# Kernel optimization log

Hardware: AMD Instinct MI355X
Metric: run time of the kernel (lower is better)

## Reference

```python
import jax, jax.numpy as jnp
import numpy as np

B, L, H, W, C = 8, 512, 768, 12, 25
S = L * W          # span_idx count, reshaped to [B, L, W, H]
Hh = H // 2        # per-direction LSTM hidden (bidirectional)


def setup_inputs() -> dict:
    key = jax.random.key(0)
    ks = jax.random.split(key, 24)
    p = lambda k, shape: jax.random.normal(k, shape, jnp.float32) * 0.02
    z = lambda n: jnp.zeros((n,), jnp.float32)
    return {
        "we": jax.random.normal(ks[0], (B, L, H), jnp.float32),
        "mask": jnp.ones((B, L), jnp.int32),
        "span_idx": jax.random.randint(ks[1], (B, S, 2), 0, L, jnp.int32),
        "pe": jax.random.normal(ks[2], (B, C, H), jnp.float32),
        # BiLSTM params (PyTorch gate order i,f,g,o)
        "w_ih_f": p(ks[3], (4 * Hh, H)), "w_hh_f": p(ks[4], (4 * Hh, Hh)),
        "b_ih_f": z(4 * Hh), "b_hh_f": z(4 * Hh),
        "w_ih_b": p(ks[5], (4 * Hh, H)), "w_hh_b": p(ks[6], (4 * Hh, Hh)),
        "b_ih_b": z(4 * Hh), "b_hh_b": z(4 * Hh),
        # project_start MLP: H -> 4H -> H
        "start_w1": p(ks[7], (4 * H, H)), "start_b1": z(4 * H),
        "start_w2": p(ks[8], (H, 4 * H)), "start_b2": z(H),
        # project_end MLP
        "end_w1": p(ks[9], (4 * H, H)), "end_b1": z(4 * H),
        "end_w2": p(ks[10], (H, 4 * H)), "end_b2": z(H),
        # out_project MLP: 2H -> 4H -> H
        "out_w1": p(ks[11], (4 * H, 2 * H)), "out_b1": z(4 * H),
        "out_w2": p(ks[12], (H, 4 * H)), "out_b2": z(H),
        # prompt_proj MLP: H -> 4H -> H
        "pr_w1": p(ks[13], (4 * H, H)), "pr_b1": z(4 * H),
        "pr_w2": p(ks[14], (H, 4 * H)), "pr_b2": z(H),
    }


def lstm_dir(x, w_ih, w_hh, b_ih, b_hh, reverse):
    # x: [B,L,D] -> per-direction hidden sequence [B,L,Hh]
    xg = jnp.einsum('bld,gd->blg', x, w_ih) + b_ih  # precomputed input gates
    n = w_hh.shape[1]

    def step(carry, xg_t):
        h, c = carry
        g = xg_t + h @ w_hh.T + b_hh
        i, f, gg, o = jnp.split(g, 4, axis=-1)
        c = jax.nn.sigmoid(f) * c + jax.nn.sigmoid(i) * jnp.tanh(gg)
        h = jax.nn.sigmoid(o) * jnp.tanh(c)
        return (h, c), h

    init = (jnp.zeros((x.shape[0], n), x.dtype), jnp.zeros((x.shape[0], n), x.dtype))
    _, hs = jax.lax.scan(step, init, jnp.swapaxes(xg, 0, 1), reverse=reverse)
    return jnp.swapaxes(hs, 0, 1)


def mlp(x, w1, b1, w2, b2):
    # Linear -> ReLU -> (Dropout: identity in eval) -> Linear
    return jax.nn.relu(x @ w1.T + b1) @ w2.T + b2


def extract_elements(t, idx):
    # t: [B,L,D], idx: [B,S] -> [B,S,D]; indices clamped like torch
    idx = jnp.clip(idx, 0, t.shape[1] - 1)
    return jnp.take_along_axis(t, idx[..., None], axis=1)


def reference(we, mask, span_idx, pe,
              w_ih_f, w_hh_f, b_ih_f, b_hh_f,
              w_ih_b, w_hh_b, b_ih_b, b_hh_b,
              start_w1, start_b1, start_w2, start_b2,
              end_w1, end_b1, end_w2, end_b2,
              out_w1, out_b1, out_w2, out_b2,
              pr_w1, pr_b1, pr_w2, pr_b2):
    # 1) Bidirectional LSTM encoder (pad_packed zeros masked positions)
    hf = lstm_dir(we, w_ih_f, w_hh_f, b_ih_f, b_hh_f, reverse=False)
    hb = lstm_dir(we, w_ih_b, w_hh_b, b_ih_b, b_hh_b, reverse=True)
    h = jnp.concatenate([hf, hb], axis=-1) * mask[..., None].astype(we.dtype)
    # 2) SpanMarkerV0: dual MLP -> gather -> concat+relu -> out MLP
    start_rep = mlp(h, start_w1, start_b1, start_w2, start_b2)
    end_rep = mlp(h, end_w1, end_b1, end_w2, end_b2)
    ss = extract_elements(start_rep, span_idx[:, :, 0])
    es = extract_elements(end_rep, span_idx[:, :, 1])
    cat = jax.nn.relu(jnp.concatenate([ss, es], axis=-1))
    span = mlp(cat, out_w1, out_b1, out_w2, out_b2).reshape(B, L, W, H)
    # 3) Prompt projection
    prompt = mlp(pe, pr_w1, pr_b1, pr_w2, pr_b2)
    return (span, prompt)
```

## Files before the change

### kernel.cpp

```cpp
#include <hip/hip_runtime.h>
#include <hip/hip_bf16.h>
#include <stdint.h>

#define B_ 8
#define L_ 512
#define H_ 768
#define WW_ 12
#define C_ 25
#define S_ (L_*WW_)
#define HH 384
#define G4 1536

using bf16x8 = __attribute__((ext_vector_type(8))) short;
using f32x4  = __attribute__((ext_vector_type(4))) float;

static __device__ __forceinline__ unsigned short f2bf(float x){
  unsigned u = __float_as_uint(x);
  unsigned r = (u + 0x7FFFu + ((u >> 16) & 1u)) >> 16;
  return (unsigned short)r;
}
static __device__ __forceinline__ float bflo(unsigned u){ return __uint_as_float(u << 16); }
static __device__ __forceinline__ float bfhi(unsigned u){ return __uint_as_float(u & 0xFFFF0000u); }

static __device__ __forceinline__ float sigmoid_f(float x){
  x = fminf(15.f, fmaxf(-15.f, x));
  return 1.f / (1.f + __expf(-x));
}
static __device__ __forceinline__ float tanh_f(float x){
  x = fminf(15.f, fmaxf(-15.f, x));
  float e = __expf(-2.f * x);
  return (1.f - e) / (1.f + e);
}

static __device__ __forceinline__ void gl_lds16(const unsigned short* g, unsigned short* l){
  __builtin_amdgcn_global_load_lds(
      (const __attribute__((address_space(1))) unsigned int*)g,
      (__attribute__((address_space(3))) unsigned int*)l,
      16, 0, 0);
}

struct CastArgs {
  const float* s[14];
  unsigned short* d[14];
  long cum[15];
};

__global__ __launch_bounds__(256) void k_cast_multi(CastArgs a, long total){
  long i = (long)blockIdx.x * blockDim.x + threadIdx.x;
  if (i >= total) return;
  int seg = 0;
  while (i >= a.cum[seg + 1]) seg++;
  long j = i - a.cum[seg];
  float4 v = reinterpret_cast<const float4*>(a.s[seg])[j];
  ushort4 o;
  o.x = f2bf(v.x); o.y = f2bf(v.y); o.z = f2bf(v.z); o.w = f2bf(v.w);
  reinterpret_cast<ushort4*>(a.d[seg])[j] = o;
}

__global__ void k_biascomb(const float* __restrict__ a, const float* __restrict__ b,
                           float* __restrict__ o, int n){
  int i = blockIdx.x * blockDim.x + threadIdx.x;
  if (i < n) o[i] = a[i] + b[i];
}

template<int ACT, int OUTBF, int GX = 0>
__global__ __launch_bounds__(256) void k_gemm2(
    const unsigned short* __restrict__ A, const unsigned short* __restrict__ Bm,
    const float* __restrict__ bias, void* __restrict__ Cout,
    int M, int N, int K, int lda, int ldb)
{
  __shared__ unsigned short Al[128 * 64];
  __shared__ unsigned short Bl[128 * 64];

  const int tid  = threadIdx.x;
  const int lane = tid & 63;
  const int wave = tid >> 6;
  const int wr = wave >> 1, wc = wave & 1;
  const int l16 = lane & 15, lq = lane >> 4;
  const int m0 = (GX == 0 ? blockIdx.y : blockIdx.x) * 128;
  const int n0 = (GX == 0 ? blockIdx.x : blockIdx.y) * 128;

  const int r_ = tid >> 3;
  const int p_ = tid & 7;
  const int cS = ((p_ ^ (r_ & 7)) * 8);
  const unsigned short* Asrc[4];
  const unsigned short* Bsrc[4];
  #pragma unroll
  for (int i = 0; i < 4; i++){
    int ra = m0 + i * 32 + r_; ra = ra < M ? ra : (M - 1);
    Asrc[i] = A + (size_t)ra * lda + cS;
    int rb = n0 + i * 32 + r_; rb = rb < N ? rb : (N - 1);
    Bsrc[i] = Bm + (size_t)rb * ldb + cS;
  }

  f32x4 acc[4][4];
  #pragma unroll
  for (int a = 0; a < 4; a++)
    #pragma unroll
    for (int b = 0; b < 4; b++)
      acc[a][b] = (f32x4)0.f;

  const int sw0 = ((0 * 4 + lq) ^ (l16 & 7)) * 16;
  const int sw1 = ((1 * 4 + lq) ^ (l16 & 7)) * 16;
  const int aBase = (wr * 64 + l16) * 128;
  const int bBase = (wc * 64 + l16) * 128;

  for (int k0 = 0; k0 < K; k0 += 64){
    #pragma unroll
    for (int i = 0; i < 4; i++)
      gl_lds16(Asrc[i] + k0, Al + i * 2048 + tid * 8);
    #pragma unroll
    for (int i = 0; i < 4; i++)
      gl_lds16(Bsrc[i] + k0, Bl + i * 2048 + tid * 8);
    __syncthreads();

    #pragma unroll
    for (int kk = 0; kk < 2; kk++){
      const int sw = kk ? sw1 : sw0;
      bf16x8 av[4], bv[4];
      #pragma unroll
      for (int mi = 0; mi < 4; mi++)
        av[mi] = *reinterpret_cast<const bf16x8*>((const char*)Al + aBase + mi * 2048 + sw);
      #pragma unroll
      for (int ni = 0; ni < 4; ni++)
        bv[ni] = *reinterpret_cast<const bf16x8*>((const char*)Bl + bBase + ni * 2048 + sw);
      #pragma unroll
      for (int mi = 0; mi < 4; mi++)
        #pragma unroll
        for (int ni = 0; ni < 4; ni++)
          acc[mi][ni] = __builtin_amdgcn_mfma_f32_16x16x32_bf16(av[mi], bv[ni], acc[mi][ni], 0, 0, 0);
    }
    __syncthreads();
  }

  #pragma unroll
  for (int mi = 0; mi < 4; mi++){
    #pragma unroll
    for (int r = 0; r < 4; r++){
      int row = m0 + wr * 64 + mi * 16 + lq * 4 + r;
      if (row >= M) continue;
      #pragma unroll
      for (int ni = 0; ni < 4; ni++){
        int col = n0 + wc * 64 + ni * 16 + l16;
        float v = acc[mi][ni][r] + bias[col];
        if (ACT) v = v > 0.f ? v : 0.f;
        if (OUTBF) ((unsigned short*)Cout)[(size_t)row * N + col] = f2bf(v);
        else       ((float*)Cout)[(size_t)row * N + col] = v;
      }
    }
  }
}

__global__ __launch_bounds__(256) void k_gout(
    const unsigned short* __restrict__ Ps, const unsigned short* __restrict__ Pe,
    const int* __restrict__ sidx, const float* __restrict__ b1,
    const unsigned short* __restrict__ Bw, const float* __restrict__ b2,
    float* __restrict__ out)
{
  __shared__ unsigned short Al[128 * 64];
  __shared__ unsigned short Bl[128 * 64];
  __shared__ int idx2[128][2];

  const int tid  = threadIdx.x;
  const int lane = tid & 63;
  const int wave = tid >> 6;
  const int wr = wave >> 1, wc = wave & 1;
  const int l16 = lane & 15, lq = lane >> 4;

  const int wg   = blockIdx.x;
  const int xcd  = wg & 7;
  const int slot = wg >> 3;
  const int nblk = slot % 6;
  const int tm   = xcd + 8 * (slot / 6);
  const int b  = tm / 48;
  const int s0 = (tm % 48) * 128;
  const int n0 = nblk * 128;

  if (tid < 128){
    int s = s0 + tid;
    int i0 = sidx[((size_t)b * S_ + s) * 2 + 0];
    int i1 = sidx[((size_t)b * S_ + s) * 2 + 1];
    idx2[tid][0] = min(max(i0, 0), L_ - 1);
    idx2[tid][1] = min(max(i1, 0), L_ - 1);
  }
  __syncthreads();

  const int r_ = tid >> 3;
  const int p_ = tid & 7;
  const int cS = ((p_ ^ (r_ & 7)) * 8);
  const unsigned short* Bsrc[4];
  const unsigned short* As0[4];
  const unsigned short* As1[4];
  #pragma unroll
  for (int i = 0; i < 4; i++){
    Bsrc[i] = Bw + (size_t)(n0 + i * 32 + r_) * 3072 + cS;
    int rr = i * 32 + r_;
    As0[i] = Ps + (size_t)(b * L_ + idx2[rr][0]) * 3072 + cS;
    As1[i] = Pe + (size_t)(b * L_ + idx2[rr][1]) * 3072 + cS;
  }

  f32x4 acc[4][4];
  #pragma unroll
  for (int a = 0; a < 4; a++)
    #pragma unroll
    for (int c = 0; c < 4; c++)
      acc[a][c] = (f32x4)0.f;

  const int sw0 = ((0 * 4 + lq) ^ (l16 & 7)) * 16;
  const int sw1 = ((1 * 4 + lq) ^ (l16 & 7)) * 16;
  const int aBase = (wr * 64 + l16) * 128;
  const int bBase = (wc * 64 + l16) * 128;

  uint4 vaR[4], veR[4];
  float4 bbR0, bbR1;
  #pragma unroll
  for (int i = 0; i < 4; i++){
    vaR[i] = *reinterpret_cast<const uint4*>(As0[i]);
    veR[i] = *reinterpret_cast<const uint4*>(As1[i]);
  }
  bbR0 = *reinterpret_cast<const float4*>(b1 + cS);
  bbR1 = *reinterpret_cast<const float4*>(b1 + cS + 4);

  for (int k0 = 0; k0 < 3072; k0 += 64){
    #pragma unroll
    for (int i = 0; i < 4; i++)
      gl_lds16(Bsrc[i] + k0, Bl + i * 2048 + tid * 8);

    #pragma unroll
    for (int i = 0; i < 4; i++){
      uint4 va = vaR[i];
      uint4 ve = veR[i];
      float f[8];
      f[0] = bflo(va.x) + bflo(ve.x) + bbR0.x; f[1] = bfhi(va.x) + bfhi(ve.x) + bbR0.y;
      f[2] = bflo(va.y) + bflo(ve.y) + bbR0.z; f[3] = bfhi(va.y) + bfhi(ve.y) + bbR0.w;
      f[4] = bflo(va.z) + bflo(ve.z) + bbR1.x; f[5] = bfhi(va.z) + bfhi(ve.z) + bbR1.y;
      f[6] = bflo(va.w) + bflo(ve.w) + bbR1.z; f[7] = bfhi(va.w) + bfhi(ve.w) + bbR1.w;
      unsigned short e[8];
      #pragma unroll
      for (int j = 0; j < 8; j++){ float v = f[j] > 0.f ? f[j] : 0.f; e[j] = f2bf(v); }
      uint4 rr;
      rr.x = (unsigned)e[0] | ((unsigned)e[1] << 16);
      rr.y = (unsigned)e[2] | ((unsigned)e[3] << 16);
      rr.z = (unsigned)e[4] | ((unsigned)e[5] << 16);
      rr.w = (unsigned)e[6] | ((unsigned)e[7] << 16);
      *reinterpret_cast<uint4*>(Al + i * 2048 + tid * 8) = rr;
    }

    if (k0 + 64 < 3072){
      #pragma unroll
      for (int i = 0; i < 4; i++){
        vaR[i] = *reinterpret_cast<const uint4*>(As0[i] + k0 + 64);
        veR[i] = *reinterpret_cast<const uint4*>(As1[i] + k0 + 64);
      }
      bbR0 = *reinterpret_cast<const float4*>(b1 + k0 + 64 + cS);
      bbR1 = *reinterpret_cast<const float4*>(b1 + k0 + 64 + cS + 4);
    }
    __syncthreads();

    #pragma unroll
    for (int kk = 0; kk < 2; kk++){
      const int sw = kk ? sw1 : sw0;
      bf16x8 av[4], bv[4];
      #pragma unroll
      for (int mi = 0; mi < 4; mi++)
        av[mi] = *reinterpret_cast<const bf16x8*>((const char*)Al + aBase + mi * 2048 + sw);
      #pragma unroll
      for (int ni = 0; ni < 4; ni++)
        bv[ni] = *reinterpret_cast<const bf16x8*>((const char*)Bl + bBase + ni * 2048 + sw);
      #pragma unroll
      for (int mi = 0; mi < 4; mi++)
        #pragma unroll
        for (int ni = 0; ni < 4; ni++)
          acc[mi][ni] = __builtin_amdgcn_mfma_f32_16x16x32_bf16(av[mi], bv[ni], acc[mi][ni], 0, 0, 0);
    }
    __syncthreads();
  }

  #pragma unroll
  for (int mi = 0; mi < 4; mi++){
    #pragma unroll
    for (int r = 0; r < 4; r++){
      size_t row = (size_t)tm * 128 + wr * 64 + mi * 16 + lq * 4 + r;
      #pragma unroll
      for (int ni = 0; ni < 4; ni++){
        int col = n0 + wc * 64 + ni * 16 + l16;
        out[row * 768 + col] = acc[mi][ni][r] + b2[col];
      }
    }
  }
}

static __device__ __forceinline__ unsigned long long ald8(const unsigned long long* p){
  return __hip_atomic_load(p, __ATOMIC_RELAXED, __HIP_MEMORY_SCOPE_AGENT);
}

__global__ __launch_bounds__(512, 2) void k_lstm7(
    const float* __restrict__ xgc,
    const unsigned short* __restrict__ Wbf,
    const int* __restrict__ mask,
    unsigned short* __restrict__ hbf,
    unsigned int* __restrict__ hg)
{
  const int dir  = blockIdx.x / 6;
  const int part = blockIdx.x % 6;
  const int tid  = threadIdx.x;
  const int lane = tid & 63;
  const int w    = tid >> 6;
  const int l16  = lane & 15, lq = lane >> 4;

  __shared__ alignas(16) unsigned short hls[8 * HH];
  __shared__ float gsl[256 * 9];

  const float* xg = xgc + dir * 1536;
  const unsigned short* Wg = Wbf + (size_t)dir * G4 * HH;
  unsigned int* hgd = hg + dir * 2 * (8 * HH);

  bf16x8 bfr0[12], bfr1[12];
  {
    int r0 = w * 32 + l16;
    int r1 = w * 32 + 16 + l16;
    int g0 = r0 >> 6, j0u = r0 & 63;
    int g1 = r1 >> 6, j1u = r1 & 63;
    const unsigned short* p0 = Wg + ((size_t)g0 * HH + part * 64 + j0u) * HH + lq * 8;
    const unsigned short* p1 = Wg + ((size_t)g1 * HH + part * 64 + j1u) * HH + lq * 8;
    #pragma unroll
    for (int kf = 0; kf < 12; kf++){
      bfr0[kf] = *reinterpret_cast<const bf16x8*>(p0 + kf * 32);
      bfr1[kf] = *reinterpret_cast<const bf16x8*>(p1 + kf * 32);
    }
  }

  if (tid < 384) reinterpret_cast<uint4*>(hls)[tid] = uint4{0,0,0,0};

  const int cb = tid >> 6;
  const int cj = tid & 63;
  const int cu = part * 64 + cj;
  float c_state = 0.f;

  const int w0  = tid * 6;
  const int rb  = w0 / HH;
  const int ru  = w0 % HH;

  float xi, xf, xgg, xo, mvf;
  {
    const int t0 = dir ? (L_ - 1) : 0;
    const float* xr = xgc + dir * 1536 + ((size_t)cb * L_ + t0) * 3072;
    xi = xr[cu]; xf = xr[HH + cu]; xgg = xr[2 * HH + cu]; xo = xr[3 * HH + cu];
    mvf = (float)mask[cb * L_ + t0];
  }

  __syncthreads();

  for (int s = 0; s < L_; s++){
    const int t = dir ? (L_ - 1 - s) : s;

    float nxi = 0.f, nxf = 0.f, nxg = 0.f, nxo = 0.f, nmv = 0.f;
    if (s + 1 < L_){
      const int tn = dir ? (L_ - 2 - s) : (s + 1);
      const float* xr = xg + ((size_t)cb * L_ + tn) * 3072;
      nxi = xr[cu]; nxf = xr[HH + cu]; nxg = xr[2 * HH + cu]; nxo = xr[3 * HH + cu];
      nmv = (float)mask[cb * L_ + tn];
    }

    if (s > 0){
      const unsigned long long tg = (unsigned long long)s;
      const unsigned long long* P =
        reinterpret_cast<const unsigned long long*>(hgd + ((s - 1) & 1) * (8 * HH) + w0);
      unsigned long long v0 = ald8(P), v1 = ald8(P + 1), v2 = ald8(P + 2);
      for (;;){
        bool ok0 = (((v0 >> 16) & 0xFFFFull) == tg) & ((v0 >> 48) == tg);
        bool ok1 = (((v1 >> 16) & 0xFFFFull) == tg) & ((v1 >> 48) == tg);
        bool ok2 = (((v2 >> 16) & 0xFFFFull) == tg) & ((v2 >> 48) == tg);
        if (ok0 & ok1 & ok2) break;
        v0 = ald8(P); v1 = ald8(P + 1); v2 = ald8(P + 2);
      }
      unsigned p01 = (unsigned)(v0 & 0xFFFFu) | ((unsigned)((v0 >> 32) & 0xFFFFu) << 16);
      unsigned p23 = (unsigned)(v1 & 0xFFFFu) | ((unsigned)((v1 >> 32) & 0xFFFFu) << 16);
      unsigned p45 = (unsigned)(v2 & 0xFFFFu) | ((unsigned)((v2 >> 32) & 0xFFFFu) << 16);
      *reinterpret_cast<unsigned*>((char*)hls + ((rb * 768 + (ru    ) * 2) ^ (rb << 4))) = p01;
      *reinterpret_cast<unsigned*>((char*)hls + ((rb * 768 + (ru + 2) * 2) ^ (rb << 4))) = p23;
      *reinterpret_cast<unsigned*>((char*)hls + ((rb * 768 + (ru + 4) * 2) ^ (rb << 4))) = p45;
    }
    __syncthreads();

    f32x4 acc0 = (f32x4)0.f, acc1 = (f32x4)0.f;
    const int arow = l16 & 7;
    #pragma unroll
    for (int kf = 0; kf < 12; kf++){
      int by = (arow * 768 + kf * 64 + lq * 16) ^ (arow << 4);
      bf16x8 a = *reinterpret_cast<const bf16x8*>((const char*)hls + by);
      acc0 = __builtin_amdgcn_mfma_f32_16x16x32_bf16(a, bfr0[kf], acc0, 0, 0, 0);
      acc1 = __builtin_amdgcn_mfma_f32_16x16x32_bf16(a, bfr1[kf], acc1, 0, 0, 0);
    }
    if (lq < 2){
      int n0r = w * 32 + l16;
      int n1r = w * 32 + 16 + l16;
      #pragma unroll
      for (int r = 0; r < 4; r++){
        gsl[n0r * 9 + lq * 4 + r] = acc0[r];
        gsl[n1r * 9 + lq * 4 + r] = acc1[r];
      }
    }
    __syncthreads();

    {
      float gi = gsl[(0 * 64 + cj) * 9 + cb] + xi;
      float gf = gsl[(1 * 64 + cj) * 9 + cb] + xf;
      float gg = gsl[(2 * 64 + cj) * 9 + cb] + xgg;
      float go = gsl[(3 * 64 + cj) * 9 + cb] + xo;
      c_state = sigmoid_f(gf) * c_state + sigmoid_f(gi) * tanh_f(gg);
      float h = sigmoid_f(go) * tanh_f(c_state);
      unsigned short hb = f2bf(h);
      *reinterpret_cast<unsigned short*>((char*)hls + ((cb * 768 + cu * 2) ^ (cb << 4))) = hb;
      unsigned word = ((unsigned)(s + 1) << 16) | (unsigned)hb;
      __hip_atomic_store(&hgd[(s & 1) * (8 * HH) + cb * HH + cu], word,
                         __ATOMIC_RELAXED, __HIP_MEMORY_SCOPE_AGENT);
      hbf[((size_t)cb * L_ + t) * H_ + dir * HH + cu] = f2bf(h * mvf);
    }

    xi = nxi; xf = nxf; xgg = nxg; xo = nxo; mvf = nmv;
  }
}

extern "C" void kernel_launch(void* const* d_in, const int* in_sizes, int n_in,
                              void* d_out, int out_size, void* d_ws, size_t ws_size,
                              hipStream_t stream)
{
  (void)in_sizes; (void)n_in; (void)out_size; (void)ws_size;
  const float* we     = (const float*)d_in[0];
  const int*   mask   = (const int*)  d_in[1];
  const int*   sidx   = (const int*)  d_in[2];
  const float* pe     = (const float*)d_in[3];
  const float* w_ih_f = (const float*)d_in[4];
  const float* w_hh_f = (const float*)d_in[5];
  const float* b_ih_f = (const float*)d_in[6];
  const float* b_hh_f = (const float*)d_in[7];
  const float* w_ih_b = (const float*)d_in[8];
  const float* w_hh_b = (const float*)d_in[9];
  const float* b_ih_b = (const float*)d_in[10];
  const float* b_hh_b = (const float*)d_in[11];
  const float* sw1 = (const float*)d_in[12]; const float* sb1 = (const float*)d_in[13];
  const float* sw2 = (const float*)d_in[14]; const float* sb2 = (const float*)d_in[15];
  const float* ew1 = (const float*)d_in[16]; const float* eb1 = (const float*)d_in[17];
  const float* ew2 = (const float*)d_in[18]; const float* eb2 = (const float*)d_in[19];
  const float* ow1 = (const float*)d_in[20]; const float* ob1 = (const float*)d_in[21];
  const float* ow2 = (const float*)d_in[22]; const float* ob2 = (const float*)d_in[23];
  const float* pw1 = (const float*)d_in[24]; const float* pb1 = (const float*)d_in[25];
  const float* pw2 = (const float*)d_in[26]; const float* pb2 = (const float*)d_in[27];

  char* wsp = (char*)d_ws; size_t off = 0;
  auto alloc = [&](size_t bytes) -> void* {
    void* p = wsp + off;
    off += (bytes + 255) & ~(size_t)255;
    return p;
  };

  unsigned short* we_bf  = (unsigned short*)alloc((size_t)4096*768*2);
  unsigned short* wihc_bf= (unsigned short*)alloc((size_t)3072*768*2);
  float* bcc   = (float*)alloc((size_t)3072*4);
  float* zerob = (float*)alloc((size_t)3072*4);
  float* sbe1  = (float*)alloc((size_t)6144*4);
  float* xgc   = (float*)alloc((size_t)4096*3072*4);
  unsigned short* whh_bf = (unsigned short*)alloc((size_t)2*1536*384*2);
  unsigned int* hg = (unsigned int*)alloc((size_t)2*2*8*384*4);
  unsigned short* h_bf  = (unsigned short*)alloc((size_t)4096*768*2);
  unsigned short* swe1b = (unsigned short*)alloc((size_t)6144*768*2);
  unsigned short* sw2b  = (unsigned short*)alloc((size_t)768*3072*2);
  unsigned short* ew2b  = (unsigned short*)alloc((size_t)768*3072*2);
  unsigned short* ow1b  = (unsigned short*)alloc((size_t)3072*1536*2);
  unsigned short* ow2b  = (unsigned short*)alloc((size_t)768*3072*2);
  unsigned short* pw1b  = (unsigned short*)alloc((size_t)3072*768*2);
  unsigned short* pw2b  = (unsigned short*)alloc((size_t)768*3072*2);
  unsigned short* srep  = (unsigned short*)alloc((size_t)4096*768*2);
  unsigned short* erep  = (unsigned short*)alloc((size_t)4096*768*2);
  unsigned short* midc  = (unsigned short*)alloc((size_t)4096*6144*2);
  unsigned short* pe_bf = (unsigned short*)alloc((size_t)200*768*2);
  unsigned short* pmid  = (unsigned short*)alloc((size_t)200*3072*2);

  unsigned short* Ps = (unsigned short*)xgc;
  unsigned short* Pe = (unsigned short*)xgc + (size_t)4096*3072;

  hipMemsetAsync(hg, 0, (size_t)2*2*8*384*4, stream);
  hipMemsetAsync(zerob, 0, (size_t)3072*4, stream);
  hipMemcpyAsync(sbe1,        sb1, (size_t)3072*4, hipMemcpyDeviceToDevice, stream);
  hipMemcpyAsync(sbe1 + 3072, eb1, (size_t)3072*4, hipMemcpyDeviceToDevice, stream);

  {
    CastArgs ca;
    const float* srcs[14] = { we, w_ih_f, w_ih_b, w_hh_f, w_hh_b, sw1, ew1,
                              sw2, ew2, ow1, ow2, pw1, pw2, pe };
    unsigned short* dsts[14] = { we_bf, wihc_bf, wihc_bf + 1536*768,
                                 whh_bf, whh_bf + 1536*384,
                                 swe1b, swe1b + 3072*768,
                                 sw2b, ew2b, ow1b, ow2b, pw1b, pw2b, pe_bf };
    long n4s[14] = { 4096L*768/4, 1536L*768/4, 1536L*768/4,
                     1536L*384/4, 1536L*384/4,
                     3072L*768/4, 3072L*768/4,
                     768L*3072/4, 768L*3072/4, 3072L*1536/4, 768L*3072/4,
                     3072L*768/4, 768L*3072/4, 200L*768/4 };
    long c = 0;
    for (int i = 0; i < 14; i++){ ca.s[i] = srcs[i]; ca.d[i] = dsts[i]; ca.cum[i] = c; c += n4s[i]; }
    ca.cum[14] = c;
    int grid = (int)((c + 255) / 256);
    k_cast_multi<<<grid, 256, 0, stream>>>(ca, c);
  }

  k_biascomb<<<6, 256, 0, stream>>>(b_ih_f, b_hh_f, bcc, 1536);
  k_biascomb<<<6, 256, 0, stream>>>(b_ih_b, b_hh_b, bcc + 1536, 1536);

  dim3 blk(256);
  k_gemm2<0,0><<<dim3(24, 32), blk, 0, stream>>>(we_bf, wihc_bf, bcc, xgc, 4096, 3072, 768, 768, 768);

  k_lstm7<<<12, 512, 0, stream>>>(xgc, whh_bf, mask, h_bf, hg);

  k_gemm2<1,1><<<dim3(48, 32), blk, 0, stream>>>(h_bf, swe1b, sbe1, midc, 4096, 6144, 768, 768, 768);
  k_gemm2<1,1,1><<<dim3(32, 6), blk, 0, stream>>>(midc,        sw2b, sb2, srep, 4096, 768, 3072, 6144, 3072);
  k_gemm2<1,1,1><<<dim3(32, 6), blk, 0, stream>>>(midc + 3072, ew2b, eb2, erep, 4096, 768, 3072, 6144, 3072);

  k_gemm2<0,1><<<dim3(24, 32), blk, 0, stream>>>(srep, ow1b,       zerob, Ps, 4096, 3072, 768, 768, 1536);
  k_gemm2<0,1><<<dim3(24, 32), blk, 0, stream>>>(erep, ow1b + 768, zerob, Pe, 4096, 3072, 768, 768, 1536);

  float* outp = (float*)d_out;
  k_gout<<<2304, blk, 0, stream>>>(Ps, Pe, sidx, ob1, ow2b, ob2, outp);

  k_gemm2<1,1><<<dim3(24, 2), blk, 0, stream>>>(pe_bf, pw1b, pb1, pmid, 200, 3072, 768, 768, 768);
  k_gemm2<0,0><<<dim3( 6, 2), blk, 0, stream>>>(pmid, pw2b, pb2,
                                                outp + (size_t)37748736, 200, 768, 3072, 3072, 3072);
}
```

Measured before the change: 1.837 ms.

## Widen span-output GEMM tile to 128x256 and batch paired GEMM launches

The gather+out-MLP kernel now uses 512 threads, each block covering a 128x256 output tile (8 waves). Each gathered A tile is therefore built once per two 128-column slices instead of twice, which halves the gather and ReLU-conversion work. The register prefetch of the next A chunk is removed, so A loads are no longer overlapped with compute. Separately, the paired start/end GEMMs are merged into single launches through a z grid dimension, and the two bias-combine kernels are merged into one, cutting launch count.

```diff
diff --git a/kernel.cpp b/kernel.cpp
--- a/kernel.cpp
+++ b/kernel.cpp
@@ -57,14 +57,16 @@
   reinterpret_cast<ushort4*>(a.d[seg])[j] = o;
 }
 
-__global__ void k_biascomb(const float* __restrict__ a, const float* __restrict__ b,
-                           float* __restrict__ o, int n){
+__global__ void k_biascomb2(const float* __restrict__ bihf, const float* __restrict__ bhhf,
+                            const float* __restrict__ bihb, const float* __restrict__ bhhb,
+                            float* __restrict__ o){
   int i = blockIdx.x * blockDim.x + threadIdx.x;
-  if (i < n) o[i] = a[i] + b[i];
-}
-
-template<int ACT, int OUTBF, int GX = 0>
-__global__ __launch_bounds__(256) void k_gemm2(
+  if (i < 1536) o[i] = bihf[i] + bhhf[i];
+  else if (i < 3072) o[i] = bihb[i - 1536] + bhhb[i - 1536];
+}
+
+template<int ACT, int OUTBF, int GX>
+static __device__ __forceinline__ void gemm2_body(
     const unsigned short* __restrict__ A, const unsigned short* __restrict__ Bm,
     const float* __restrict__ bias, void* __restrict__ Cout,
     int M, int N, int K, int lda, int ldb)
@@ -151,30 +153,55 @@
   }
 }
 
-__global__ __launch_bounds__(256) void k_gout(
+template<int ACT, int OUTBF, int GX = 0>
+__global__ __launch_bounds__(256) void k_gemm2(
+    const unsigned short* A, const unsigned short* Bm,
+    const float* bias, void* Cout, int M, int N, int K, int lda, int ldb)
+{
+  gemm2_body<ACT, OUTBF, GX>(A, Bm, bias, Cout, M, N, K, lda, ldb);
+}
+
+struct GemmPair {
+  const unsigned short *A0, *A1, *B0, *B1;
+  const float *b0, *b1;
+  void *C0, *C1;
+};
+
+template<int ACT, int OUTBF, int GX = 0>
+__global__ __launch_bounds__(256) void k_gemm2z(
+    GemmPair p, int M, int N, int K, int lda, int ldb)
+{
+  const int z = blockIdx.z;
+  gemm2_body<ACT, OUTBF, GX>(z ? p.A1 : p.A0, z ? p.B1 : p.B0,
+                             z ? p.b1 : p.b0, z ? p.C1 : p.C0,
+                             M, N, K, lda, ldb);
+}
+
+__global__ __launch_bounds__(512, 4) void k_gout(
     const unsigned short* __restrict__ Ps, const unsigned short* __restrict__ Pe,
     const int* __restrict__ sidx, const float* __restrict__ b1,
     const unsigned short* __restrict__ Bw, const float* __restrict__ b2,
     float* __restrict__ out)
 {
   __shared__ unsigned short Al[128 * 64];
-  __shared__ unsigned short Bl[128 * 64];
+  __shared__ unsigned short Bl[256 * 64];
   __shared__ int idx2[128][2];
 
   const int tid  = threadIdx.x;
   const int lane = tid & 63;
   const int wave = tid >> 6;
-  const int wr = wave >> 1, wc = wave & 1;
+  const int wr = wave >> 2;
+  const int wc = wave & 3;
   const int l16 = lane & 15, lq = lane >> 4;
 
   const int wg   = blockIdx.x;
   const int xcd  = wg & 7;
   const int slot = wg >> 3;
-  const int nblk = slot % 6;
-  const int tm   = xcd + 8 * (slot / 6);
+  const int nblk = slot % 3;
+  const int tm   = xcd + 8 * (slot / 3);
   const int b  = tm / 48;
   const int s0 = (tm % 48) * 128;
-  const int n0 = nblk * 128;
+  const int n0 = nblk * 256;
 
   if (tid < 128){
     int s = s0 + tid;
@@ -189,12 +216,14 @@
   const int p_ = tid & 7;
   const int cS = ((p_ ^ (r_ & 7)) * 8);
   const unsigned short* Bsrc[4];
-  const unsigned short* As0[4];
-  const unsigned short* As1[4];
-  #pragma unroll
-  for (int i = 0; i < 4; i++){
-    Bsrc[i] = Bw + (size_t)(n0 + i * 32 + r_) * 3072 + cS;
-    int rr = i * 32 + r_;
+  const unsigned short* As0[2];
+  const unsigned short* As1[2];
+  #pragma unroll
+  for (int i = 0; i < 4; i++)
+    Bsrc[i] = Bw + (size_t)(n0 + i * 64 + r_) * 3072 + cS;
+  #pragma unroll
+  for (int i = 0; i < 2; i++){
+    int rr = i * 64 + r_;
     As0[i] = Ps + (size_t)(b * L_ + idx2[rr][0]) * 3072 + cS;
     As1[i] = Pe + (size_t)(b * L_ + idx2[rr][1]) * 3072 + cS;
   }
@@ -211,30 +240,21 @@
   const int aBase = (wr * 64 + l16) * 128;
   const int bBase = (wc * 64 + l16) * 128;
 
-  uint4 vaR[4], veR[4];
-  float4 bbR0, bbR1;
-  #pragma unroll
-  for (int i = 0; i < 4; i++){
-    vaR[i] = *reinterpret_cast<const uint4*>(As0[i]);
-    veR[i] = *reinterpret_cast<const uint4*>(As1[i]);
-  }
-  bbR0 = *reinterpret_cast<const float4*>(b1 + cS);
-  bbR1 = *reinterpret_cast<const float4*>(b1 + cS + 4);
-
   for (int k0 = 0; k0 < 3072; k0 += 64){
     #pragma unroll
     for (int i = 0; i < 4; i++)
-      gl_lds16(Bsrc[i] + k0, Bl + i * 2048 + tid * 8);
-
-    #pragma unroll
-    for (int i = 0; i < 4; i++){
-      uint4 va = vaR[i];
-      uint4 ve = veR[i];
+      gl_lds16(Bsrc[i] + k0, Bl + i * 4096 + tid * 8);
+    float4 bb0 = *reinterpret_cast<const float4*>(b1 + k0 + cS);
+    float4 bb1 = *reinterpret_cast<const float4*>(b1 + k0 + cS + 4);
+    #pragma unroll
+    for (int i = 0; i < 2; i++){
+      uint4 va = *reinterpret_cast<const uint4*>(As0[i] + k0);
+      uint4 ve = *reinterpret_cast<const uint4*>(As1[i] + k0);
       float f[8];
-      f[0] = bflo(va.x) + bflo(ve.x) + bbR0.x; f[1] = bfhi(va.x) + bfhi(ve.x) + bbR0.y;
-      f[2] = bflo(va.y) + bflo(ve.y) + bbR0.z; f[3] = bfhi(va.y) + bfhi(ve.y) + bbR0.w;
-      f[4] = bflo(va.z) + bflo(ve.z) + bbR1.x; f[5] = bfhi(va.z) + bfhi(ve.z) + bbR1.y;
-      f[6] = bflo(va.w) + bflo(ve.w) + bbR1.z; f[7] = bfhi(va.w) + bfhi(ve.w) + bbR1.w;
+      f[0] = bflo(va.x) + bflo(ve.x) + bb0.x; f[1] = bfhi(va.x) + bfhi(ve.x) + bb0.y;
+      f[2] = bflo(va.y) + bflo(ve.y) + bb0.z; f[3] = bfhi(va.y) + bfhi(ve.y) + bb0.w;
+      f[4] = bflo(va.z) + bflo(ve.z) + bb1.x; f[5] = bfhi(va.z) + bfhi(ve.z) + bb1.y;
+      f[6] = bflo(va.w) + bflo(ve.w) + bb1.z; f[7] = bfhi(va.w) + bfhi(ve.w) + bb1.w;
       unsigned short e[8];
       #pragma unroll
       for (int j = 0; j < 8; j++){ float v = f[j] > 0.f ? f[j] : 0.f; e[j] = f2bf(v); }
@@ -243,17 +263,7 @@
       rr.y = (unsigned)e[2] | ((unsigned)e[3] << 16);
       rr.z = (unsigned)e[4] | ((unsigned)e[5] << 16);
       rr.w = (unsigned)e[6] | ((unsigned)e[7] << 16);
-      *reinterpret_cast<uint4*>(Al + i * 2048 + tid * 8) = rr;
-    }
-
-    if (k0 + 64 < 3072){
-      #pragma unroll
-      for (int i = 0; i < 4; i++){
-        vaR[i] = *reinterpret_cast<const uint4*>(As0[i] + k0 + 64);
-        veR[i] = *reinterpret_cast<const uint4*>(As1[i] + k0 + 64);
-      }
-      bbR0 = *reinterpret_cast<const float4*>(b1 + k0 + 64 + cS);
-      bbR1 = *reinterpret_cast<const float4*>(b1 + k0 + 64 + cS + 4);
+      *reinterpret_cast<uint4*>(Al + i * 4096 + tid * 8) = rr;
     }
     __syncthreads();
 
@@ -344,7 +354,7 @@
   float xi, xf, xgg, xo, mvf;
   {
     const int t0 = dir ? (L_ - 1) : 0;
-    const float* xr = xgc + dir * 1536 + ((size_t)cb * L_ + t0) * 3072;
+    const float* xr = xg + ((size_t)cb * L_ + t0) * 3072;
     xi = xr[cu]; xf = xr[HH + cu]; xgg = xr[2 * HH + cu]; xo = xr[3 * HH + cu];
     mvf = (float)mask[cb * L_ + t0];
   }
@@ -505,8 +515,7 @@
     k_cast_multi<<<grid, 256, 0, stream>>>(ca, c);
   }
 
-  k_biascomb<<<6, 256, 0, stream>>>(b_ih_f, b_hh_f, bcc, 1536);
-  k_biascomb<<<6, 256, 0, stream>>>(b_ih_b, b_hh_b, bcc + 1536, 1536);
+  k_biascomb2<<<12, 256, 0, stream>>>(b_ih_f, b_hh_f, b_ih_b, b_hh_b, bcc);
 
   dim3 blk(256);
   k_gemm2<0,0><<<dim3(24, 32), blk, 0, stream>>>(we_bf, wihc_bf, bcc, xgc, 4096, 3072, 768, 768, 768);
@@ -514,14 +523,23 @@
   k_lstm7<<<12, 512, 0, stream>>>(xgc, whh_bf, mask, h_bf, hg);
 
   k_gemm2<1,1><<<dim3(48, 32), blk, 0, stream>>>(h_bf, swe1b, sbe1, midc, 4096, 6144, 768, 768, 768);
-  k_gemm2<1,1,1><<<dim3(32, 6), blk, 0, stream>>>(midc,        sw2b, sb2, srep, 4096, 768, 3072, 6144, 3072);
-  k_gemm2<1,1,1><<<dim3(32, 6), blk, 0, stream>>>(midc + 3072, ew2b, eb2, erep, 4096, 768, 3072, 6144, 3072);
-
-  k_gemm2<0,1><<<dim3(24, 32), blk, 0, stream>>>(srep, ow1b,       zerob, Ps, 4096, 3072, 768, 768, 1536);
-  k_gemm2<0,1><<<dim3(24, 32), blk, 0, stream>>>(erep, ow1b + 768, zerob, Pe, 4096, 3072, 768, 768, 1536);
+
+  {
+    GemmPair p;
+    p.A0 = midc;        p.B0 = sw2b; p.b0 = sb2; p.C0 = srep;
+    p.A1 = midc + 3072; p.B1 = ew2b; p.b1 = eb2; p.C1 = erep;
+    k_gemm2z<1,1,1><<<dim3(32, 6, 2), blk, 0, stream>>>(p, 4096, 768, 3072, 6144, 3072);
+  }
+
+  {
+    GemmPair p;
+    p.A0 = srep; p.B0 = ow1b;       p.b0 = zerob; p.C0 = Ps;
+    p.A1 = erep; p.B1 = ow1b + 768; p.b1 = zerob; p.C1 = Pe;
+    k_gemm2z<0,1,0><<<dim3(24, 32, 2), blk, 0, stream>>>(p, 4096, 3072, 768, 768, 1536);
+  }
 
   float* outp = (float*)d_out;
-  k_gout<<<2304, blk, 0, stream>>>(Ps, Pe, sidx, ob1, ow2b, ob2, outp);
+  k_gout<<<1152, dim3(512), 0, stream>>>(Ps, Pe, sidx, ob1, ow2b, ob2, outp);
 
   k_gemm2<1,1><<<dim3(24, 2), blk, 0, stream>>>(pe_bf, pw1b, pb1, pmid, 200, 3072, 768, 768, 768);
   k_gemm2<0,0><<<dim3( 6, 2), blk, 0, stream>>>(pmid, pw2b, pb2,
```

New measurement: 1.683 ms, median of 2. 1.09x faster.
